# Performance work log

Measured on AMD Instinct MI355X. Metric: run time of the kernel, lower is better.

## Reference

```python
import jax, jax.numpy as jnp
import numpy as np
import math

DIM = 2048
N_HEADS = 32
N_KV_HEADS = 8
HEAD_DIM = DIM // N_HEADS  # 64
N_REP = N_HEADS // N_KV_HEADS  # 4
BATCH = 1
SEQ = 2048


def rope_cos_sin(seq_len, head_dim, dtype=jnp.float32):
    inv_freq = 1.0 / (10000.0 ** (jnp.arange(0, head_dim, 2, dtype=jnp.float32) / head_dim))
    t = jnp.arange(seq_len, dtype=jnp.float32)
    freqs = jnp.outer(t, inv_freq)            # [S, D/2]
    emb = jnp.concatenate([freqs, freqs], -1)  # [S, D]
    return jnp.cos(emb).astype(dtype), jnp.sin(emb).astype(dtype)


def rotate_half(x):
    x1 = x[..., ::2]
    x2 = x[..., 1::2]
    return jnp.concatenate([-x2, x1], axis=-1)


def setup_inputs() -> dict:
    key = jax.random.key(0)
    ks = jax.random.split(key, 5)
    scale = 1.0 / math.sqrt(DIM)
    x = jax.random.normal(ks[0], (BATCH, SEQ, DIM), jnp.float32)
    wq = jax.random.normal(ks[1], (DIM, N_HEADS * HEAD_DIM), jnp.float32) * scale
    wk = jax.random.normal(ks[2], (DIM, N_KV_HEADS * HEAD_DIM), jnp.float32) * scale
    wv = jax.random.normal(ks[3], (DIM, N_KV_HEADS * HEAD_DIM), jnp.float32) * scale
    wo = jax.random.normal(ks[4], (N_HEADS * HEAD_DIM, DIM), jnp.float32) * scale
    mask = jnp.tril(jnp.ones((SEQ, SEQ), jnp.int32))[None, None]  # [1,1,S,S]
    return {"x": x, "mask": mask, "wq": wq, "wk": wk, "wv": wv, "wo": wo}


def reference(x, mask, wq, wk, wv, wo):
    B, S, _ = x.shape
    q = (x @ wq).reshape(B, S, N_HEADS, HEAD_DIM).transpose(0, 2, 1, 3)     # [B,H,S,D]
    k = (x @ wk).reshape(B, S, N_KV_HEADS, HEAD_DIM).transpose(0, 2, 1, 3)  # [B,Hkv,S,D]
    v = (x @ wv).reshape(B, S, N_KV_HEADS, HEAD_DIM).transpose(0, 2, 1, 3)
    cos, sin = rope_cos_sin(S, HEAD_DIM)  # [S,D]
    q = q * cos + rotate_half(q) * sin
    k = k * cos + rotate_half(k) * sin
    if N_REP > 1:
        k = jnp.repeat(k, N_REP, axis=1)
        v = jnp.repeat(v, N_REP, axis=1)
    scores = jnp.einsum("bhqd,bhkd->bhqk", q, k) / math.sqrt(HEAD_DIM)
    scores = jnp.where(mask == 0, -jnp.inf, scores)
    attn = jax.nn.softmax(scores, axis=-1)
    out = jnp.einsum("bhqk,bhkd->bhqd", attn, v)  # [B,H,S,D]
    out = out.transpose(0, 2, 1, 3).reshape(B, S, N_HEADS * HEAD_DIM)
    return out @ wo
```

## Files before the change

kernel.cpp:

```cpp
#include <hip/hip_runtime.h>
#include <hip/hip_bf16.h>

#define DIM 2048
#define SEQ 2048
#define NH 32
#define HD 64
#define NKV 8
#define QKV_LD 3072

typedef __attribute__((ext_vector_type(8))) short bf16x8;
typedef __attribute__((ext_vector_type(4))) float f32x4;
typedef __attribute__((ext_vector_type(2))) unsigned int uint2v;
typedef unsigned short ushort_t;

__device__ inline unsigned short f2bf(float f) {
    union { float f; unsigned int u; } v; v.f = f;
    unsigned int r = v.u + 0x7fffu + ((v.u >> 16) & 1u);
    return (unsigned short)(r >> 16);
}
__device__ inline float bf2f(ushort_t u) {
    union { unsigned int u; float f; } v; v.u = ((unsigned int)u) << 16; return v.f;
}

__device__ inline void async_cp16(const void* g, void* l) {
    __builtin_amdgcn_global_load_lds(
        (const __attribute__((address_space(1))) unsigned int*)g,
        (__attribute__((address_space(3))) unsigned int*)l, 16, 0, 0);
}

__device__ inline void pswap32(unsigned int& a, unsigned int& b) {
    uint2v r = __builtin_amdgcn_permlane32_swap(a, b, false, false);
    a = r[0]; b = r[1];
}
__device__ inline void pswap16(unsigned int& a, unsigned int& b) {
    uint2v r = __builtin_amdgcn_permlane16_swap(a, b, false, false);
    a = r[0]; b = r[1];
}
__device__ inline float wave_max(float x) {
    unsigned int a = __float_as_uint(x), b = a;
    uint2v r = __builtin_amdgcn_permlane16_swap(a, b, false, false);
    x = fmaxf(__uint_as_float(r[0]), __uint_as_float(r[1]));
    a = __float_as_uint(x); b = a;
    r = __builtin_amdgcn_permlane32_swap(a, b, false, false);
    return fmaxf(__uint_as_float(r[0]), __uint_as_float(r[1]));
}
__device__ inline float wave_sum(float x) {
    unsigned int a = __float_as_uint(x), b = a;
    uint2v r = __builtin_amdgcn_permlane16_swap(a, b, false, false);
    x = __uint_as_float(r[0]) + __uint_as_float(r[1]);
    a = __float_as_uint(x); b = a;
    r = __builtin_amdgcn_permlane32_swap(a, b, false, false);
    return __uint_as_float(r[0]) + __uint_as_float(r[1]);
}
__device__ inline unsigned int cvt_pk_bf16(float lo, float hi) {
    unsigned int r;
    asm volatile("v_cvt_pk_bf16_f32 %0, %1, %2" : "=v"(r) : "v"(lo), "v"(hi));
    return r;
}

__global__ __launch_bounds__(256) void convert_kernel(
    const float* __restrict__ X, ushort_t* __restrict__ Xb)
{
    int i = (blockIdx.x * 256 + threadIdx.x) * 4;
    float4 v = *(const float4*)(X + i);
    ushort_t o[4] = { f2bf(v.x), f2bf(v.y), f2bf(v.z), f2bf(v.w) };
    *(uint2*)(Xb + i) = *(uint2*)o;
}

__global__ __launch_bounds__(256) void transpose_kernel(
    const float* __restrict__ W, ushort_t* __restrict__ WT, int N)
{
    __shared__ __align__(16) ushort_t tile[64][72];
    const int n0 = blockIdx.x * 64, k0 = blockIdx.y * 64;
    const int t = threadIdx.x;
    {
        const int tk = t >> 4;
        const int tn = (t & 15) * 4;
        #pragma unroll
        for (int i = 0; i < 4; i++) {
            const int k = tk + i * 16;
            float4 v = *(const float4*)(W + (size_t)(k0 + k) * N + n0 + tn);
            tile[tn + 0][k] = f2bf(v.x);
            tile[tn + 1][k] = f2bf(v.y);
            tile[tn + 2][k] = f2bf(v.z);
            tile[tn + 3][k] = f2bf(v.w);
        }
    }
    __syncthreads();
    {
        const int tn = t >> 2;
        const int tk = (t & 3) * 16;
        uint4 a = *(const uint4*)&tile[tn][tk];
        uint4 b = *(const uint4*)&tile[tn][tk + 8];
        ushort_t* dst = WT + (size_t)(n0 + tn) * DIM + k0 + tk;
        *(uint4*)dst = a;
        *(uint4*)(dst + 8) = b;
    }
}

template<int OUT_F32>
__global__ __launch_bounds__(256) void gemm_kernel(
    const ushort_t* __restrict__ A, const ushort_t* __restrict__ BT,
    void* __restrict__ Cout, int K, int lda, int ldo)
{
    __shared__ __align__(16) ushort_t sA[128 * 32];
    __shared__ __align__(16) ushort_t sB[128 * 32];
    const int tn = blockIdx.x * 128, tm = blockIdx.y * 128;
    const int t = threadIdx.x, wave = t >> 6, lane = t & 63;
    const int m16 = lane & 15, quad = lane >> 4;
    const int wr = (wave >> 1) * 64, wc = (wave & 1) * 64;
    const int srow = lane >> 2;
    const int sce = (lane & 3) * 8;

    f32x4 acc[4][4] = {};

    for (int k0 = 0; k0 < K; k0 += 32) {
        __syncthreads();
        #pragma unroll
        for (int p = 0; p < 2; p++) {
            const int j = wave * 2 + p;
            const int row = j * 16 + srow;
            async_cp16(A  + (size_t)(tm + row) * lda + k0 + sce, &sA[j * 512]);
            async_cp16(BT + (size_t)(tn + row) * K   + k0 + sce, &sB[j * 512]);
        }
        __syncthreads();
        bf16x8 af[4], bf[4];
        #pragma unroll
        for (int mt = 0; mt < 4; mt++)
            af[mt] = *(const bf16x8*)&sA[(wr + mt * 16 + m16) * 32 + quad * 8];
        #pragma unroll
        for (int nt = 0; nt < 4; nt++)
            bf[nt] = *(const bf16x8*)&sB[(wc + nt * 16 + m16) * 32 + quad * 8];
        #pragma unroll
        for (int mt = 0; mt < 4; mt++)
            #pragma unroll
            for (int nt = 0; nt < 4; nt++)
                acc[mt][nt] = __builtin_amdgcn_mfma_f32_16x16x32_bf16(af[mt], bf[nt], acc[mt][nt], 0, 0, 0);
    }

    #pragma unroll
    for (int mt = 0; mt < 4; mt++) {
        const int row = tm + wr + mt * 16 + quad * 4;
        #pragma unroll
        for (int nt = 0; nt < 4; nt++) {
            const int col = tn + wc + nt * 16 + m16;
            #pragma unroll
            for (int r = 0; r < 4; r++) {
                if (OUT_F32)
                    ((float*)Cout)[(size_t)(row + r) * ldo + col] = acc[mt][nt][r];
                else
                    ((ushort_t*)Cout)[(size_t)(row + r) * ldo + col] = f2bf(acc[mt][nt][r]);
            }
        }
    }
}

#define QSCALE 0.18033688011112042f
__global__ __launch_bounds__(256) void rope_kernel(ushort_t* qkv, ushort_t* __restrict__ Kr)
{
    const int gid = blockIdx.x * 256 + threadIdx.x;
    const int lane = gid & 63;
    const int idx = gid >> 6;
    const int s = idx / 40;
    const int hh = idx - s * 40;

    const ushort_t* src;
    ushort_t* dst;
    const bool isq = (hh < 32);
    if (isq) {
        dst = qkv + (size_t)s * QKV_LD + hh * 64;
        src = dst;
    } else {
        src = qkv + (size_t)s * QKV_LD + 2048 + (hh - 32) * 64;
        dst = Kr + ((size_t)(hh - 32) * SEQ + s) * 64;
    }

    const float e = bf2f(src[lane]);
    const int i = lane & 31;
    const float freq = __expf(-(float)i * 0.28782313662425572f);
    const float ang = (float)s * freq;
    const float cv = cosf(ang), sv = sinf(ang);
    const int partner = (lane < 32) ? (2 * lane + 1) : (2 * (lane - 32));
    const float y = __shfl(e, partner, 64);
    float out = (lane < 32) ? (e * cv - y * sv) : (e * cv + y * sv);
    if (isq) out *= QSCALE;
    dst[lane] = f2bf(out);
}

__global__ __launch_bounds__(256) void vtrans_kernel(
    const ushort_t* __restrict__ qkv, ushort_t* __restrict__ Vt)
{
    __shared__ __align__(16) ushort_t tile[64][72];
    const int kvh = blockIdx.x & 7;
    const int s0 = (blockIdx.x >> 3) * 64;
    const int t = threadIdx.x;
    {
        const int sr = t >> 3;
        const int d8 = (t & 7) * 8;
        #pragma unroll
        for (int i = 0; i < 2; i++) {
            const int s = sr + i * 32;
            ushort_t tmp[8];
            *(uint4*)tmp = *(const uint4*)(qkv + (size_t)(s0 + s) * QKV_LD + 2560 + kvh * 64 + d8);
            #pragma unroll
            for (int j = 0; j < 8; j++) tile[d8 + j][s] = tmp[j];
        }
    }
    __syncthreads();
    {
        const int dr = t >> 3;
        const int s8 = (t & 7) * 8;
        #pragma unroll
        for (int i = 0; i < 2; i++) {
            const int d = dr + i * 32;
            *(uint4*)(Vt + ((size_t)kvh * 64 + d) * SEQ + s0 + s8) = *(const uint4*)&tile[d][s8];
        }
    }
}

__global__ __launch_bounds__(512, 2) void attn_kernel(
    ushort_t* qkv, const ushort_t* __restrict__ Kr, const ushort_t* __restrict__ Vt)
{
    const int t = threadIdx.x, wave = t >> 6, lane = t & 63;
    const int m16 = lane & 15, quad = lane >> 4;
    const int h = blockIdx.x & 31;
    const int p = blockIdx.x >> 5;
    const int grp = wave >> 2;
    const int w4 = wave & 3;
    const int band = grp ? p : 15 - p;
    const int kvh = h >> 2;

    const ushort_t* Krh = Kr + (size_t)kvh * SEQ * 64;
    const ushort_t* Vth = Vt + (size_t)kvh * 64 * SEQ;

    const int nkt = band * 2 + 2;

    int qi[2];
    bf16x8 qf[2][2];
    #pragma unroll
    for (int qa = 0; qa < 2; qa++) {
        qi[qa] = band * 128 + (w4 + qa * 4) * 16 + m16;
        const ushort_t* qp = qkv + (size_t)qi[qa] * QKV_LD + h * 64 + quad * 8;
        qf[qa][0] = *(const bf16x8*)qp;
        qf[qa][1] = *(const bf16x8*)(qp + 32);
    }

    f32x4 oacc[2][4] = {};
    float m_run[2] = { -1e30f, -1e30f };
    float l_run[2] = { 0.f, 0.f };

    bf16x8 kf[4][2];
    #pragma unroll
    for (int knt = 0; knt < 4; knt++) {
        const ushort_t* kp = Krh + (size_t)(knt * 16 + m16) * 64 + quad * 8;
        kf[knt][0] = *(const bf16x8*)kp;
        kf[knt][1] = *(const bf16x8*)(kp + 32);
    }

    for (int kt = 0; kt < nkt; kt++) {
        const int kbase = kt * 64;
        const bool last = (kt == nkt - 1);

        f32x4 sc[2][4] = {};
        __builtin_amdgcn_s_setprio(1);
        #pragma unroll
        for (int qa = 0; qa < 2; qa++) {
            if (qa == 0 && last) continue;
            #pragma unroll
            for (int knt = 0; knt < 4; knt++) {
                sc[qa][knt] = __builtin_amdgcn_mfma_f32_16x16x32_bf16(kf[knt][0], qf[qa][0], sc[qa][knt], 0, 0, 0);
                sc[qa][knt] = __builtin_amdgcn_mfma_f32_16x16x32_bf16(kf[knt][1], qf[qa][1], sc[qa][knt], 0, 0, 0);
            }
        }
        __builtin_amdgcn_s_setprio(0);

        bf16x8 vf[4][2];
        #pragma unroll
        for (int nt = 0; nt < 4; nt++) {
            const ushort_t* vp = Vth + (size_t)(nt * 16 + m16) * SEQ + kbase + quad * 8;
            vf[nt][0] = *(const bf16x8*)vp;
            vf[nt][1] = *(const bf16x8*)(vp + 32);
        }
        if (!last) {
            #pragma unroll
            for (int knt = 0; knt < 4; knt++) {
                const ushort_t* kp = Krh + (size_t)(kbase + 64 + knt * 16 + m16) * 64 + quad * 8;
                kf[knt][0] = *(const bf16x8*)kp;
                kf[knt][1] = *(const bf16x8*)(kp + 32);
            }
        }

        #pragma unroll
        for (int qa = 0; qa < 2; qa++) {
            if (qa == 0 && last) continue;
            const bool domask = (qa == 0) ? (kt == nkt - 2) : last;

            float s[16];
            #pragma unroll
            for (int knt = 0; knt < 4; knt++)
                #pragma unroll
                for (int r = 0; r < 4; r++) {
                    float v = sc[qa][knt][r];
                    if (domask && (kbase + knt * 16 + quad * 4 + r > qi[qa])) v = -1e30f;
                    s[knt * 4 + r] = v;
                }

            float x0 = fmaxf(s[0], s[1]),  x1 = fmaxf(s[2], s[3]);
            float x2 = fmaxf(s[4], s[5]),  x3 = fmaxf(s[6], s[7]);
            float x4 = fmaxf(s[8], s[9]),  x5 = fmaxf(s[10], s[11]);
            float x6 = fmaxf(s[12], s[13]), x7 = fmaxf(s[14], s[15]);
            float rmax = fmaxf(fmaxf(fmaxf(x0, x1), fmaxf(x2, x3)),
                               fmaxf(fmaxf(x4, x5), fmaxf(x6, x7)));
            rmax = wave_max(rmax);

            if (rmax > m_run[qa] + 8.f) {
                const float mnew = fmaxf(m_run[qa], rmax);
                const float alpha = __builtin_amdgcn_exp2f(m_run[qa] - mnew);
                m_run[qa] = mnew;
                l_run[qa] *= alpha;
                #pragma unroll
                for (int nt = 0; nt < 4; nt++)
                    #pragma unroll
                    for (int r = 0; r < 4; r++) oacc[qa][nt][r] *= alpha;
            }
            const float m = m_run[qa];

            #pragma unroll
            for (int i = 0; i < 16; i++) s[i] = __builtin_amdgcn_exp2f(s[i] - m);
            float y0 = s[0] + s[1],  y1 = s[2] + s[3];
            float y2 = s[4] + s[5],  y3 = s[6] + s[7];
            float y4 = s[8] + s[9],  y5 = s[10] + s[11];
            float y6 = s[12] + s[13], y7 = s[14] + s[15];
            float ps = ((y0 + y1) + (y2 + y3)) + ((y4 + y5) + (y6 + y7));
            l_run[qa] += wave_sum(ps);

            unsigned int u00 = cvt_pk_bf16(s[0],  s[1]),  u01 = cvt_pk_bf16(s[2],  s[3]);
            unsigned int u10 = cvt_pk_bf16(s[4],  s[5]),  u11 = cvt_pk_bf16(s[6],  s[7]);
            unsigned int u20 = cvt_pk_bf16(s[8],  s[9]),  u21 = cvt_pk_bf16(s[10], s[11]);
            unsigned int u30 = cvt_pk_bf16(s[12], s[13]), u31 = cvt_pk_bf16(s[14], s[15]);
            pswap32(u00, u10); pswap16(u00, u10);
            pswap32(u01, u11); pswap16(u01, u11);
            pswap32(u20, u30); pswap16(u20, u30);
            pswap32(u21, u31); pswap16(u21, u31);
            union { unsigned int w[4]; bf16x8 v; } P0, P1;
            P0.w[0] = u00; P0.w[1] = u01; P0.w[2] = u10; P0.w[3] = u11;
            P1.w[0] = u20; P1.w[1] = u21; P1.w[2] = u30; P1.w[3] = u31;

            __builtin_amdgcn_s_setprio(1);
            #pragma unroll
            for (int nt = 0; nt < 4; nt++) {
                oacc[qa][nt] = __builtin_amdgcn_mfma_f32_16x16x32_bf16(vf[nt][0], P0.v, oacc[qa][nt], 0, 0, 0);
                oacc[qa][nt] = __builtin_amdgcn_mfma_f32_16x16x32_bf16(vf[nt][1], P1.v, oacc[qa][nt], 0, 0, 0);
            }
            __builtin_amdgcn_s_setprio(0);
        }
    }

    #pragma unroll
    for (int qa = 0; qa < 2; qa++) {
        const float rl = 1.f / l_run[qa];
        #pragma unroll
        for (int nt = 0; nt < 4; nt++) {
            ushort_t pk[4];
            #pragma unroll
            for (int r = 0; r < 4; r++) pk[r] = f2bf(oacc[qa][nt][r] * rl);
            *(uint2*)&qkv[(size_t)qi[qa] * QKV_LD + h * 64 + nt * 16 + quad * 4] = *(uint2*)pk;
        }
    }
}

extern "C" void kernel_launch(void* const* d_in, const int* in_sizes, int n_in,
                              void* d_out, int out_size, void* d_ws, size_t ws_size,
                              hipStream_t stream)
{
    const float* x  = (const float*)d_in[0];
    const float* wq = (const float*)d_in[2];
    const float* wk = (const float*)d_in[3];
    const float* wv = (const float*)d_in[4];
    const float* wo = (const float*)d_in[5];

    ushort_t* WT  = (ushort_t*)d_ws;
    ushort_t* xb  = WT + (size_t)3072 * 2048;
    ushort_t* woT = xb;
    ushort_t* qkv = xb + (size_t)2048 * 2048;
    ushort_t* Kr  = qkv + (size_t)SEQ * QKV_LD;
    ushort_t* Vt  = Kr + (size_t)NKV * SEQ * HD;

    dim3 blk(256);

    convert_kernel<<<(DIM * SEQ) / 1024, blk, 0, stream>>>(x, xb);
    transpose_kernel<<<dim3(32, 32), blk, 0, stream>>>(wq, WT, 2048);
    transpose_kernel<<<dim3(8, 32),  blk, 0, stream>>>(wk, WT + (size_t)2048 * 2048, 512);
    transpose_kernel<<<dim3(8, 32),  blk, 0, stream>>>(wv, WT + (size_t)2560 * 2048, 512);

    gemm_kernel<0><<<dim3(QKV_LD / 128, SEQ / 128), blk, 0, stream>>>(xb, WT, qkv, DIM, DIM, QKV_LD);

    transpose_kernel<<<dim3(32, 32), blk, 0, stream>>>(wo, woT, 2048);

    rope_kernel<<<(SEQ * 40 * 64) / 256, blk, 0, stream>>>(qkv, Kr);
    vtrans_kernel<<<NKV * (SEQ / 64), blk, 0, stream>>>(qkv, Vt);

    attn_kernel<<<8 * NH, dim3(512), 0, stream>>>(qkv, Kr, Vt);

    gemm_kernel<1><<<dim3(DIM / 128, SEQ / 128), blk, 0, stream>>>(qkv, woT, d_out, DIM, QKV_LD, DIM);
}
```

Measured before the change: 300.4 us.

## Unroll attention key loop by two with ping-pong K registers and kv-head-grouped block order

The attention key-tile loop is unrolled by two, using two K register buffers (kfA/kfB) that alternate so the loop-carried register copy goes away and the last-tile checks become compile-time. Block indices are also remapped so consecutive blocks share the same KV head, aiming for better L2 reuse of K and V across the four query heads of a group. The unroll raises register pressure under launch_bounds(512,2) and may cause spills. The last pair also loads K for one tile past the causal range, which stays within the buffer.

```diff
diff --git a/kernel.cpp b/kernel.cpp
--- a/kernel.cpp
+++ b/kernel.cpp
@@ -218,17 +218,104 @@
     }
 }
 
+#define MFMA16(A, B, C) __builtin_amdgcn_mfma_f32_16x16x32_bf16(A, B, C, 0, 0, 0)
+
+#define LOADK(KF, KB) do { \
+    _Pragma("unroll") \
+    for (int _k = 0; _k < 4; _k++) { \
+        const ushort_t* _kp = Krh + (size_t)((KB) + _k * 16 + m16) * 64 + quad * 8; \
+        KF[_k][0] = *(const bf16x8*)_kp; \
+        KF[_k][1] = *(const bf16x8*)(_kp + 32); \
+    } \
+} while (0)
+
+#define LOADV(VF, KB) do { \
+    _Pragma("unroll") \
+    for (int _n = 0; _n < 4; _n++) { \
+        const ushort_t* _vp = Vth + (size_t)(_n * 16 + m16) * SEQ + (KB) + quad * 8; \
+        VF[_n][0] = *(const bf16x8*)_vp; \
+        VF[_n][1] = *(const bf16x8*)(_vp + 32); \
+    } \
+} while (0)
+
+#define QKT(SC, KF, QA) do { \
+    _Pragma("unroll") \
+    for (int _k = 0; _k < 4; _k++) { \
+        SC[_k] = MFMA16(KF[_k][0], qf[QA][0], SC[_k]); \
+        SC[_k] = MFMA16(KF[_k][1], qf[QA][1], SC[_k]); \
+    } \
+} while (0)
+
+#define SMPV(SC, QA, DOMASK, KBASE, VF) do { \
+    float s_[16]; \
+    _Pragma("unroll") \
+    for (int _k = 0; _k < 4; _k++) { \
+        _Pragma("unroll") \
+        for (int _r = 0; _r < 4; _r++) { \
+            float _v = SC[_k][_r]; \
+            if ((DOMASK) && ((KBASE) + _k * 16 + quad * 4 + _r > qi[QA])) _v = -1e30f; \
+            s_[_k * 4 + _r] = _v; \
+        } \
+    } \
+    float _x0 = fmaxf(s_[0], s_[1]),   _x1 = fmaxf(s_[2], s_[3]); \
+    float _x2 = fmaxf(s_[4], s_[5]),   _x3 = fmaxf(s_[6], s_[7]); \
+    float _x4 = fmaxf(s_[8], s_[9]),   _x5 = fmaxf(s_[10], s_[11]); \
+    float _x6 = fmaxf(s_[12], s_[13]), _x7 = fmaxf(s_[14], s_[15]); \
+    float _rmax = fmaxf(fmaxf(fmaxf(_x0, _x1), fmaxf(_x2, _x3)), \
+                        fmaxf(fmaxf(_x4, _x5), fmaxf(_x6, _x7))); \
+    _rmax = wave_max(_rmax); \
+    if (_rmax > m_run[QA] + 8.f) { \
+        const float _mnew = fmaxf(m_run[QA], _rmax); \
+        const float _alpha = __builtin_amdgcn_exp2f(m_run[QA] - _mnew); \
+        m_run[QA] = _mnew; \
+        l_run[QA] *= _alpha; \
+        _Pragma("unroll") \
+        for (int _n = 0; _n < 4; _n++) { \
+            _Pragma("unroll") \
+            for (int _r = 0; _r < 4; _r++) oacc[QA][_n][_r] *= _alpha; \
+        } \
+    } \
+    const float _m = m_run[QA]; \
+    _Pragma("unroll") \
+    for (int _i = 0; _i < 16; _i++) s_[_i] = __builtin_amdgcn_exp2f(s_[_i] - _m); \
+    float _y0 = s_[0] + s_[1],   _y1 = s_[2] + s_[3]; \
+    float _y2 = s_[4] + s_[5],   _y3 = s_[6] + s_[7]; \
+    float _y4 = s_[8] + s_[9],   _y5 = s_[10] + s_[11]; \
+    float _y6 = s_[12] + s_[13], _y7 = s_[14] + s_[15]; \
+    float _ps = ((_y0 + _y1) + (_y2 + _y3)) + ((_y4 + _y5) + (_y6 + _y7)); \
+    l_run[QA] += wave_sum(_ps); \
+    unsigned int _u00 = cvt_pk_bf16(s_[0],  s_[1]),  _u01 = cvt_pk_bf16(s_[2],  s_[3]); \
+    unsigned int _u10 = cvt_pk_bf16(s_[4],  s_[5]),  _u11 = cvt_pk_bf16(s_[6],  s_[7]); \
+    unsigned int _u20 = cvt_pk_bf16(s_[8],  s_[9]),  _u21 = cvt_pk_bf16(s_[10], s_[11]); \
+    unsigned int _u30 = cvt_pk_bf16(s_[12], s_[13]), _u31 = cvt_pk_bf16(s_[14], s_[15]); \
+    pswap32(_u00, _u10); pswap16(_u00, _u10); \
+    pswap32(_u01, _u11); pswap16(_u01, _u11); \
+    pswap32(_u20, _u30); pswap16(_u20, _u30); \
+    pswap32(_u21, _u31); pswap16(_u21, _u31); \
+    union { unsigned int w[4]; bf16x8 v; } _P0, _P1; \
+    _P0.w[0] = _u00; _P0.w[1] = _u01; _P0.w[2] = _u10; _P0.w[3] = _u11; \
+    _P1.w[0] = _u20; _P1.w[1] = _u21; _P1.w[2] = _u30; _P1.w[3] = _u31; \
+    __builtin_amdgcn_s_setprio(1); \
+    _Pragma("unroll") \
+    for (int _n = 0; _n < 4; _n++) { \
+        oacc[QA][_n] = MFMA16(VF[_n][0], _P0.v, oacc[QA][_n]); \
+        oacc[QA][_n] = MFMA16(VF[_n][1], _P1.v, oacc[QA][_n]); \
+    } \
+    __builtin_amdgcn_s_setprio(0); \
+} while (0)
+
 __global__ __launch_bounds__(512, 2) void attn_kernel(
     ushort_t* qkv, const ushort_t* __restrict__ Kr, const ushort_t* __restrict__ Vt)
 {
     const int t = threadIdx.x, wave = t >> 6, lane = t & 63;
     const int m16 = lane & 15, quad = lane >> 4;
-    const int h = blockIdx.x & 31;
-    const int p = blockIdx.x >> 5;
+    const int b = blockIdx.x;
+    const int kvh = b & 7;
+    const int h = kvh * 4 + ((b >> 3) & 3);
+    const int p = b >> 5;
     const int grp = wave >> 2;
     const int w4 = wave & 3;
     const int band = grp ? p : 15 - p;
-    const int kvh = h >> 2;
 
     const ushort_t* Krh = Kr + (size_t)kvh * SEQ * 64;
     const ushort_t* Vth = Vt + (size_t)kvh * 64 * SEQ;
@@ -249,110 +336,40 @@
     float m_run[2] = { -1e30f, -1e30f };
     float l_run[2] = { 0.f, 0.f };
 
-    bf16x8 kf[4][2];
-    #pragma unroll
-    for (int knt = 0; knt < 4; knt++) {
-        const ushort_t* kp = Krh + (size_t)(knt * 16 + m16) * 64 + quad * 8;
-        kf[knt][0] = *(const bf16x8*)kp;
-        kf[knt][1] = *(const bf16x8*)(kp + 32);
-    }
-
-    for (int kt = 0; kt < nkt; kt++) {
-        const int kbase = kt * 64;
-        const bool last = (kt == nkt - 1);
-
-        f32x4 sc[2][4] = {};
+    bf16x8 kfA[4][2], kfB[4][2], vf[4][2];
+    LOADK(kfA, 0);
+
+    for (int kt = 0; kt < nkt; kt += 2) {
+        const bool lastpair = (kt == nkt - 2);
+        const int kb0 = kt * 64, kb1 = kb0 + 64;
+
+        f32x4 scA0[4] = {}, scA1[4] = {};
         __builtin_amdgcn_s_setprio(1);
-        #pragma unroll
-        for (int qa = 0; qa < 2; qa++) {
-            if (qa == 0 && last) continue;
-            #pragma unroll
-            for (int knt = 0; knt < 4; knt++) {
-                sc[qa][knt] = __builtin_amdgcn_mfma_f32_16x16x32_bf16(kf[knt][0], qf[qa][0], sc[qa][knt], 0, 0, 0);
-                sc[qa][knt] = __builtin_amdgcn_mfma_f32_16x16x32_bf16(kf[knt][1], qf[qa][1], sc[qa][knt], 0, 0, 0);
-            }
-        }
+        QKT(scA0, kfA, 0);
+        QKT(scA1, kfA, 1);
         __builtin_amdgcn_s_setprio(0);
-
-        bf16x8 vf[4][2];
-        #pragma unroll
-        for (int nt = 0; nt < 4; nt++) {
-            const ushort_t* vp = Vth + (size_t)(nt * 16 + m16) * SEQ + kbase + quad * 8;
-            vf[nt][0] = *(const bf16x8*)vp;
-            vf[nt][1] = *(const bf16x8*)(vp + 32);
-        }
-        if (!last) {
-            #pragma unroll
-            for (int knt = 0; knt < 4; knt++) {
-                const ushort_t* kp = Krh + (size_t)(kbase + 64 + knt * 16 + m16) * 64 + quad * 8;
-                kf[knt][0] = *(const bf16x8*)kp;
-                kf[knt][1] = *(const bf16x8*)(kp + 32);
-            }
-        }
-
-        #pragma unroll
-        for (int qa = 0; qa < 2; qa++) {
-            if (qa == 0 && last) continue;
-            const bool domask = (qa == 0) ? (kt == nkt - 2) : last;
-
-            float s[16];
-            #pragma unroll
-            for (int knt = 0; knt < 4; knt++)
-                #pragma unroll
-                for (int r = 0; r < 4; r++) {
-                    float v = sc[qa][knt][r];
-                    if (domask && (kbase + knt * 16 + quad * 4 + r > qi[qa])) v = -1e30f;
-                    s[knt * 4 + r] = v;
-                }
-
-            float x0 = fmaxf(s[0], s[1]),  x1 = fmaxf(s[2], s[3]);
-            float x2 = fmaxf(s[4], s[5]),  x3 = fmaxf(s[6], s[7]);
-            float x4 = fmaxf(s[8], s[9]),  x5 = fmaxf(s[10], s[11]);
-            float x6 = fmaxf(s[12], s[13]), x7 = fmaxf(s[14], s[15]);
-            float rmax = fmaxf(fmaxf(fmaxf(x0, x1), fmaxf(x2, x3)),
-                               fmaxf(fmaxf(x4, x5), fmaxf(x6, x7)));
-            rmax = wave_max(rmax);
-
-            if (rmax > m_run[qa] + 8.f) {
-                const float mnew = fmaxf(m_run[qa], rmax);
-                const float alpha = __builtin_amdgcn_exp2f(m_run[qa] - mnew);
-                m_run[qa] = mnew;
-                l_run[qa] *= alpha;
-                #pragma unroll
-                for (int nt = 0; nt < 4; nt++)
-                    #pragma unroll
-                    for (int r = 0; r < 4; r++) oacc[qa][nt][r] *= alpha;
-            }
-            const float m = m_run[qa];
-
-            #pragma unroll
-            for (int i = 0; i < 16; i++) s[i] = __builtin_amdgcn_exp2f(s[i] - m);
-            float y0 = s[0] + s[1],  y1 = s[2] + s[3];
-            float y2 = s[4] + s[5],  y3 = s[6] + s[7];
-            float y4 = s[8] + s[9],  y5 = s[10] + s[11];
-            float y6 = s[12] + s[13], y7 = s[14] + s[15];
-            float ps = ((y0 + y1) + (y2 + y3)) + ((y4 + y5) + (y6 + y7));
-            l_run[qa] += wave_sum(ps);
-
-            unsigned int u00 = cvt_pk_bf16(s[0],  s[1]),  u01 = cvt_pk_bf16(s[2],  s[3]);
-            unsigned int u10 = cvt_pk_bf16(s[4],  s[5]),  u11 = cvt_pk_bf16(s[6],  s[7]);
-            unsigned int u20 = cvt_pk_bf16(s[8],  s[9]),  u21 = cvt_pk_bf16(s[10], s[11]);
-            unsigned int u30 = cvt_pk_bf16(s[12], s[13]), u31 = cvt_pk_bf16(s[14], s[15]);
-            pswap32(u00, u10); pswap16(u00, u10);
-            pswap32(u01, u11); pswap16(u01, u11);
-            pswap32(u20, u30); pswap16(u20, u30);
-            pswap32(u21, u31); pswap16(u21, u31);
-            union { unsigned int w[4]; bf16x8 v; } P0, P1;
-            P0.w[0] = u00; P0.w[1] = u01; P0.w[2] = u10; P0.w[3] = u11;
-            P1.w[0] = u20; P1.w[1] = u21; P1.w[2] = u30; P1.w[3] = u31;
-
+        LOADV(vf, kb0);
+        LOADK(kfB, kb1);
+        SMPV(scA0, 0, lastpair, kb0, vf);
+        SMPV(scA1, 1, false,    kb0, vf);
+
+        if (!lastpair) {
+            f32x4 scB0[4] = {}, scB1[4] = {};
             __builtin_amdgcn_s_setprio(1);
-            #pragma unroll
-            for (int nt = 0; nt < 4; nt++) {
-                oacc[qa][nt] = __builtin_amdgcn_mfma_f32_16x16x32_bf16(vf[nt][0], P0.v, oacc[qa][nt], 0, 0, 0);
-                oacc[qa][nt] = __builtin_amdgcn_mfma_f32_16x16x32_bf16(vf[nt][1], P1.v, oacc[qa][nt], 0, 0, 0);
-            }
+            QKT(scB0, kfB, 0);
+            QKT(scB1, kfB, 1);
             __builtin_amdgcn_s_setprio(0);
+            LOADV(vf, kb1);
+            LOADK(kfA, kb1 + 64);
+            SMPV(scB0, 0, false, kb1, vf);
+            SMPV(scB1, 1, false, kb1, vf);
+        } else {
+            f32x4 scB1[4] = {};
+            __builtin_amdgcn_s_setprio(1);
+            QKT(scB1, kfB, 1);
+            __builtin_amdgcn_s_setprio(0);
+            LOADV(vf, kb1);
+            SMPV(scB1, 1, true, kb1, vf);
         }
     }
 
```

Result: no change. 301.8 us (+0.5%).
